# Kernel tuning notes

Measured on AMD Instinct MI355X. Metric: run time of the kernel, lower is better.

The kernel has to match this reference:

```python
import jax, jax.numpy as jnp
import numpy as np

PATCH = 3
PAD = PATCH // 2  # stride = 1


def _extract_patches(x):
    """torch F.unfold(k=3, s=1, p=1) reshaped to [b, n=h*w, c*3*3] (c slowest, then ki, kj)."""
    b, c, h, w = x.shape
    xp = jnp.pad(x, ((0, 0), (0, 0), (PAD, PAD), (PAD, PAD)))
    # stack the 9 shifted views -> [b, c, 9, h, w]
    pats = jnp.stack([xp[:, :, i:i + h, j:j + w]
                      for i in range(PATCH) for j in range(PATCH)], axis=2)
    pats = pats.reshape(b, c, PATCH, PATCH, h, w)
    # -> [b, h*w, c*PATCH*PATCH], matching torch unfold channel ordering
    return pats.transpose(0, 4, 5, 1, 2, 3).reshape(b, h * w, c * PATCH * PATCH)


def _l2_normalize(x):
    # F.normalize(dim=2): x / max(||x||_2, 1e-12)
    n = jnp.linalg.norm(x, axis=2, keepdims=True)
    return x / jnp.maximum(n, 1e-12)


def _fold(patches_flat, c, h, w):
    """torch F.fold(k=3, s=1, p=1): overlap-add patches back to [b, c, h, w]."""
    b = patches_flat.shape[0]
    p = patches_flat.reshape(b, h, w, c, PATCH, PATCH)
    out = jnp.zeros((b, c, h + 2 * PAD, w + 2 * PAD), patches_flat.dtype)
    for i in range(PATCH):
        for j in range(PATCH):
            out = out.at[:, :, i:i + h, j:j + w].add(
                p[:, :, :, :, i, j].transpose(0, 3, 1, 2))
    return out[:, :, PAD:PAD + h, PAD:PAD + w]


def setup_inputs() -> dict:
    key = jax.random.key(0)
    k1, k2 = jax.random.split(key)
    B, C, H, W = 1, 256, 96, 96
    return {
        "content_features": jax.random.normal(k1, (B, C, H, W), dtype=jnp.float32),
        "style_features": jax.random.normal(k2, (B, C, H, W), dtype=jnp.float32),
    }


def reference(content_features, style_features):
    b, c, h, w = content_features.shape
    cpat = _extract_patches(content_features)   # [b, n, d]
    spat = _extract_patches(style_features)     # [b, m, d]
    # all-pairs cosine similarity: [b, n, m]
    sim = jnp.einsum('bnd,bmd->bnm', _l2_normalize(cpat), _l2_normalize(spat))
    best = jnp.argmax(sim, axis=2)              # [b, n]
    matched = jnp.take_along_axis(spat, best[:, :, None], axis=1)  # [b, n, d]
    num = _fold(matched, c, h, w)
    den = _fold(jnp.ones_like(matched), c, h, w)
    return num / (den + 1e-8)
```

## Files before the change

kernel.cpp:

```cpp
#include <hip/hip_runtime.h>

#define HH 96
#define WW 96
#define CCH 256
#define NPIX (HH*WW)
#define HP 98
#define NROWS 9604
#define CORE_LO 99
#define CORE_HI 9505

typedef unsigned short u16;
typedef short bf16x8 __attribute__((ext_vector_type(8)));
typedef float f32x4 __attribute__((ext_vector_type(4)));
typedef int i32x4 __attribute__((ext_vector_type(4)));

__device__ __forceinline__ f32x4 ld4u(const float* p) {
    f32x4 r; __builtin_memcpy(&r, p, 16); return r;
}
__device__ __forceinline__ i32x4 ld4ui(const int* p) {
    i32x4 r; __builtin_memcpy(&r, p, 16); return r;
}

__device__ __forceinline__ u16 f2bf_rne(float x) {
    unsigned u = __float_as_uint(x);
    return (u16)((u + 0x7FFFu + ((u >> 16) & 1u)) >> 16);
}

__device__ __forceinline__ void stage8(const u16* const* srcs, u16* dst, int kb) {
#pragma unroll
    for (int t = 0; t < 8; ++t)
        __builtin_amdgcn_global_load_lds(
            (const __attribute__((address_space(1))) unsigned int*)(srcs[t] + kb),
            (__attribute__((address_space(3))) unsigned int*)(dst + t * 512),
            16, 0, 0);
}

__global__ __launch_bounds__(256) void tobf16_kernel(const float* __restrict__ X,
                                                     u16* __restrict__ HiT,
                                                     u16* __restrict__ LoT) {
    __shared__ u16 hi[64][65], lo[64][65];
    const int n0 = blockIdx.x * 64, k0 = blockIdx.y * 64;
    const int t = threadIdx.x;
    {
        const int kr = t >> 6, nl = t & 63;
#pragma unroll
        for (int r = 0; r < 16; ++r) {
            int kl = kr * 16 + r;
            float x = X[(k0 + kl) * NPIX + n0 + nl];
            u16 h = f2bf_rne(x);
            float hf = __uint_as_float((unsigned)h << 16);
            hi[kl][nl] = h;
            lo[kl][nl] = f2bf_rne(x - hf);
        }
    }
    __syncthreads();
    {
        const int nr = t >> 6, kl = t & 63;
#pragma unroll
        for (int r = 0; r < 16; ++r) {
            int nl = nr * 16 + r;
            HiT[(n0 + nl) * CCH + k0 + kl] = hi[kl][nl];
            LoT[(n0 + nl) * CCH + k0 + kl] = lo[kl][nl];
        }
    }
}

__global__ __launch_bounds__(256) void xst_kernel(const float* __restrict__ X,
                                                  float* __restrict__ XT) {
    __shared__ float tile[64][65];
    const int p0 = blockIdx.x * 64, c0 = blockIdx.y * 64;
    const int t = threadIdx.x;
    const int rr = t >> 6, cl = t & 63;
#pragma unroll
    for (int r = 0; r < 16; ++r)
        tile[rr * 16 + r][cl] = X[(c0 + rr * 16 + r) * NPIX + p0 + cl];
    __syncthreads();
#pragma unroll
    for (int r = 0; r < 16; ++r)
        XT[(p0 + rr * 16 + r) * CCH + c0 + cl] = tile[cl][rr * 16 + r];
}

__global__ __launch_bounds__(256) void prep_kernel(const float* __restrict__ Xs,
                                                   float* __restrict__ ssum,
                                                   unsigned long long* __restrict__ keys) {
    int p = blockIdx.x * 256 + threadIdx.x;
    if (p >= NPIX) return;
    float s = 0.f;
#pragma unroll 8
    for (int c = 0; c < CCH; ++c) {
        float v = Xs[c * NPIX + p];
        s = fmaf(v, v, s);
    }
    ssum[p] = s;
    keys[p] = 0ULL;
}

__global__ __launch_bounds__(256) void rnsbp_kernel(const float* __restrict__ ssum,
                                                    float* __restrict__ rnsp,
                                                    float* __restrict__ biasp,
                                                    int* __restrict__ midxp) {
    int mp = blockIdx.x * 256 + threadIdx.x;
    if (mp >= 9632) return;
    int yq = mp / HP, xq = mp - yq * HP;
    bool real = (yq >= 1 && yq <= 96 && xq >= 1 && xq <= 96);
    if (!real) { rnsp[mp] = 0.f; biasp[mp] = -3e38f; midxp[mp] = 0; return; }
    int y = yq - 1, x = xq - 1;
    float s = 0.f;
    for (int dy = -1; dy <= 1; ++dy) {
        int yy = y + dy;
        if ((unsigned)yy >= HH) continue;
        for (int dx = -1; dx <= 1; ++dx) {
            int xx = x + dx;
            if ((unsigned)xx >= WW) continue;
            s += ssum[yy * WW + xx];
        }
    }
    rnsp[mp] = 1.f / fmaxf(sqrtf(s), 1e-12f);
    biasp[mp] = 0.f;
    midxp[mp] = y * WW + x;
}

__global__ __launch_bounds__(256) void padzero_kernel(float* __restrict__ cc, int wstride) {
    int p = blockIdx.x;
    int yq = p / HP, xq = p - yq * HP;
    if (yq >= 1 && yq <= 96 && xq >= 1 && xq <= 96) return;
    const f32x4 z = {0.f, 0.f, 0.f, 0.f};
    float* row = cc + (long long)p * wstride;
    for (int c = threadIdx.x * 4; c < wstride; c += 1024)
        *(f32x4*)&row[c] = z;
}

__global__ __launch_bounds__(256, 2) void cc_gemm_kernel(
        const u16* __restrict__ ChiT, const u16* __restrict__ CloT,
        const u16* __restrict__ ShiT, const u16* __restrict__ SloT,
        const u16* __restrict__ zbuf,
        float* __restrict__ cc, int csp, int wstride) {
    __shared__ u16 lds[2][4][8][64][8];

    const int tid = threadIdx.x;
    const int n0 = blockIdx.x * 128;
    const int m0 = blockIdx.y * 128;
    const int wave = tid >> 6, lane = tid & 63;
    const int wr = wave >> 1, wc = wave & 1;
    const int rlo = lane & 15, kseg = (lane >> 4) * 8;

    const u16* srcs[8];
    if (wave < 2) {
        const u16* base = (wave == 0) ? ChiT : CloT;
#pragma unroll
        for (int t = 0; t < 8; ++t)
            srcs[t] = base + (n0 + t * 16 + rlo) * CCH + kseg;
    } else {
        const u16* base = (wave == 2) ? ShiT : SloT;
#pragma unroll
        for (int t = 0; t < 8; ++t) {
            int qp = csp + m0 + t * 16 + rlo;
            int yq = qp / HP, xq = qp - yq * HP;
            bool ok = (qp < NROWS) && (yq >= 1 && yq <= 96 && xq >= 1 && xq <= 96);
            srcs[t] = ok ? (base + ((yq - 1) * WW + (xq - 1)) * CCH + kseg)
                         : (zbuf + kseg);
        }
    }
    u16* slab0 = &lds[0][wave][0][0][0];
    u16* slab1 = &lds[1][wave][0][0][0];

    f32x4 acc[4][4];
#pragma unroll
    for (int i = 0; i < 4; ++i)
#pragma unroll
        for (int j = 0; j < 4; ++j) acc[i][j] = (f32x4){0.f, 0.f, 0.f, 0.f};

    stage8(srcs, slab0, 0);
    __syncthreads();

    for (int kk = 0; kk < 8; ++kk) {
        const int cur = kk & 1;
        if (kk < 7) stage8(srcs, cur ? slab0 : slab1, (kk + 1) * 32);

        bf16x8 ah[4], al[4], bh[4], bl[4];
#pragma unroll
        for (int i = 0; i < 4; ++i) {
            ah[i] = *(const bf16x8*)&lds[cur][0][wr * 4 + i][lane][0];
            al[i] = *(const bf16x8*)&lds[cur][1][wr * 4 + i][lane][0];
            bh[i] = *(const bf16x8*)&lds[cur][2][wc * 4 + i][lane][0];
            bl[i] = *(const bf16x8*)&lds[cur][3][wc * 4 + i][lane][0];
        }
#pragma unroll
        for (int i = 0; i < 4; ++i)
#pragma unroll
            for (int j = 0; j < 4; ++j) {
                acc[i][j] = __builtin_amdgcn_mfma_f32_16x16x32_bf16(ah[i], bh[j], acc[i][j], 0, 0, 0);
                acc[i][j] = __builtin_amdgcn_mfma_f32_16x16x32_bf16(ah[i], bl[j], acc[i][j], 0, 0, 0);
                acc[i][j] = __builtin_amdgcn_mfma_f32_16x16x32_bf16(al[i], bh[j], acc[i][j], 0, 0, 0);
            }
        __syncthreads();
    }

    const int r0 = (lane >> 4) * 4;
    const int cl = lane & 15;
#pragma unroll
    for (int i = 0; i < 4; ++i) {
        const int prow = n0 + wr * 64 + i * 16 + r0;
#pragma unroll
        for (int r = 0; r < 4; ++r) {
            const int row = prow + r;
            const int pp = row + 2 * (row / WW) + CORE_LO;
            const long long base = (long long)pp * wstride + m0 + wc * 64 + cl;
#pragma unroll
            for (int j = 0; j < 4; ++j)
                cc[base + j * 16] = acc[i][j][r];
        }
    }
}

__global__ __launch_bounds__(256) void boxsum_kernel(
        const float* __restrict__ cc, const float* __restrict__ rnsp,
        const float* __restrict__ biasp, const int* __restrict__ midxp,
        unsigned long long* __restrict__ keys,
        int core0, int coreEnd, int csp, int wstride) {
    const int wave = threadIdx.x >> 6, lane = threadIdx.x & 63;
    const int n = blockIdx.x * 4 + wave;
    const int pp = n + 2 * (n / WW) + CORE_LO;
    const long long rowbase = (long long)pp * wstride - csp;
    const int W1 = wstride + 1;

    const int OFF[9] = {-99, -98, -97, -1, 0, 1, 97, 98, 99};
    const float* tp[9];
#pragma unroll
    for (int t = 0; t < 9; ++t)
        tp[t] = cc + rowbase + core0 + lane * 4 + (long long)OFF[t] * W1;

    float best = -1e30f;
    int bidx = 0;
    for (int mq = core0 + lane * 4; mq < coreEnd; mq += 256) {
        f32x4 s = {0.f, 0.f, 0.f, 0.f};
#pragma unroll
        for (int t = 0; t < 9; ++t) { s += ld4u(tp[t]); tp[t] += 256; }
        f32x4 rv = ld4u(rnsp + mq);
        f32x4 bv = ld4u(biasp + mq);
        i32x4 iv = ld4ui(midxp + mq);
#pragma unroll
        for (int sl = 0; sl < 4; ++sl) {
            float v = fmaf(s[sl], rv[sl], bv[sl]);
            if (mq + sl >= coreEnd) v = -3e38f;
            if (v > best) { best = v; bidx = iv[sl]; }
        }
    }
#pragma unroll
    for (int d = 32; d; d >>= 1) {
        float ov = __shfl_xor(best, d);
        int oi = __shfl_xor(bidx, d);
        if (ov > best || (ov == best && oi < bidx)) { best = ov; bidx = oi; }
    }
    if (lane == 0) {
        unsigned u = __float_as_uint(best);
        unsigned key = (u & 0x80000000u) ? ~u : (u | 0x80000000u);
        unsigned long long k64 = ((unsigned long long)key << 32)
                               | (unsigned long long)(0xFFFFFFFFu - (unsigned)bidx);
        atomicMax(&keys[n], k64);
    }
}

__global__ __launch_bounds__(256) void fold2_kernel(const float* __restrict__ XsT,
                                                    const unsigned long long* __restrict__ keys,
                                                    float* __restrict__ outT) {
    const int wave = threadIdx.x >> 6, lane = threadIdx.x & 63;
    const int p = blockIdx.x * 4 + wave;
    const int y = p / WW, x = p - y * WW;
    f32x4 num = {0.f, 0.f, 0.f, 0.f};
    int den = 0;
#pragma unroll
    for (int i = 0; i < 3; ++i) {
        int ny = y + 1 - i;
        if ((unsigned)ny >= HH) continue;
#pragma unroll
        for (int j = 0; j < 3; ++j) {
            int nx = x + 1 - j;
            if ((unsigned)nx >= WW) continue;
            den++;
            unsigned long long k64 = keys[ny * WW + nx];
            int mg = (int)(0xFFFFFFFFu - (unsigned)(k64 & 0xFFFFFFFFu));
            int my = mg / WW, mx = mg - my * WW;
            int sy = my + i - 1, sx = mx + j - 1;
            if ((unsigned)sy < HH && (unsigned)sx < WW)
                num += ld4u(XsT + (long long)(sy * WW + sx) * CCH + lane * 4);
        }
    }
    float inv = 1.f / ((float)den + 1e-8f);
    f32x4 o = {num[0] * inv, num[1] * inv, num[2] * inv, num[3] * inv};
    *(f32x4*)&outT[(long long)p * CCH + lane * 4] = o;
}

__global__ __launch_bounds__(256) void outtr_kernel(const float* __restrict__ outT,
                                                    float* __restrict__ out) {
    __shared__ float tile[64][65];
    const int p0 = blockIdx.x * 64, c0 = blockIdx.y * 64;
    const int t = threadIdx.x;
    const int rr = t >> 6, cl = t & 63;
#pragma unroll
    for (int r = 0; r < 16; ++r)
        tile[rr * 16 + r][cl] = outT[(long long)(p0 + rr * 16 + r) * CCH + c0 + cl];
    __syncthreads();
#pragma unroll
    for (int r = 0; r < 16; ++r)
        out[(long long)(c0 + rr * 16 + r) * NPIX + p0 + cl] = tile[cl][rr * 16 + r];
}

extern "C" void kernel_launch(void* const* d_in, const int* in_sizes, int n_in,
                              void* d_out, int out_size, void* d_ws, size_t ws_size,
                              hipStream_t stream) {
    (void)in_sizes; (void)n_in; (void)out_size;
    const float* Xc = (const float*)d_in[0];
    const float* Xs = (const float*)d_in[1];
    float* out = (float*)d_out;

    char* w = (char*)d_ws;
    unsigned long long* keys = (unsigned long long*)w;  w += (size_t)NPIX * 8;
    float* ssum  = (float*)w;                           w += (size_t)NPIX * 4;
    float* rnsp  = (float*)w;                           w += (size_t)9632 * 4;
    float* biasp = (float*)w;                           w += (size_t)9632 * 4;
    int*   midxp = (int*)w;                             w += (size_t)9632 * 4;
    u16*   zbuf  = (u16*)w;                             w += 1024;
    float* XsT   = (float*)w;                           w += (size_t)NPIX * CCH * 4;
    float* outT  = (float*)w;                           w += (size_t)NPIX * CCH * 4;
    u16* ChiT = (u16*)w;                                w += (size_t)NPIX * CCH * 2;
    u16* CloT = (u16*)w;                                w += (size_t)NPIX * CCH * 2;
    u16* ShiT = (u16*)w;                                w += (size_t)NPIX * CCH * 2;
    u16* SloT = (u16*)w;                                w += (size_t)NPIX * CCH * 2;
    float* ccbuf = (float*)w;
    const size_t fixed = (size_t)(w - (char*)d_ws);

    long long avail = (ws_size > fixed + 4096)
                        ? (long long)(ws_size - fixed - 4096) : 0;
    int wstride = (int)(((avail / ((long long)NROWS * 4)) / 128) * 128);
    if (wstride > 2560) wstride = 2560;
    if (wstride < 512) wstride = 512;
    const int McCore = wstride - 198;

    hipMemsetAsync(zbuf, 0, 1024, stream);
    dim3 gt(NPIX / 64, CCH / 64);
    tobf16_kernel<<<gt, 256, 0, stream>>>(Xc, ChiT, CloT);
    tobf16_kernel<<<gt, 256, 0, stream>>>(Xs, ShiT, SloT);
    xst_kernel<<<gt, 256, 0, stream>>>(Xs, XsT);
    prep_kernel<<<NPIX / 256, 256, 0, stream>>>(Xs, ssum, keys);
    rnsbp_kernel<<<38, 256, 0, stream>>>(ssum, rnsp, biasp, midxp);
    padzero_kernel<<<NROWS, 256, 0, stream>>>(ccbuf, wstride);

    for (int core0 = CORE_LO; core0 < CORE_HI; core0 += McCore) {
        int coreEnd = (core0 + McCore < CORE_HI) ? core0 + McCore : CORE_HI;
        int csp = core0 - 99;
        int ce = coreEnd + 99; if (ce > NROWS) ce = NROWS;
        int Wc = ce - csp;
        dim3 g(NPIX / 128, (Wc + 127) / 128);
        cc_gemm_kernel<<<g, 256, 0, stream>>>(ChiT, CloT, ShiT, SloT, zbuf,
                                              ccbuf, csp, wstride);
        boxsum_kernel<<<NPIX / 4, 256, 0, stream>>>(ccbuf, rnsp, biasp, midxp, keys,
                                                    core0, coreEnd, csp, wstride);
    }

    fold2_kernel<<<NPIX / 4, 256, 0, stream>>>(XsT, keys, outT);
    outtr_kernel<<<gt, 256, 0, stream>>>(outT, out);
}
```

Measured before the change: 452.5 us.

## Prefetch two K-steps ahead with explicit vmcnt waits and split barriers

Restructures the GEMM main loop so two stages are loaded before compute begins. Each step waits on vmcnt only for the older stage, reads LDS into registers, then barriers before issuing the next async stage8 into the freed slab. The goal is to overlap global-to-LDS loads with the MFMA work and to hide more latency. The cost is hand-placed waitcnt and sched barriers, which depend on stage8 issuing exactly 8 vm ops and could break if that count changes.

```diff
diff --git a/kernel.cpp b/kernel.cpp
--- a/kernel.cpp
+++ b/kernel.cpp
@@ -171,30 +171,49 @@
         for (int j = 0; j < 4; ++j) acc[i][j] = (f32x4){0.f, 0.f, 0.f, 0.f};
 
     stage8(srcs, slab0, 0);
-    __syncthreads();
-
-    for (int kk = 0; kk < 8; ++kk) {
-        const int cur = kk & 1;
-        if (kk < 7) stage8(srcs, cur ? slab0 : slab1, (kk + 1) * 32);
-
-        bf16x8 ah[4], al[4], bh[4], bl[4];
-#pragma unroll
-        for (int i = 0; i < 4; ++i) {
-            ah[i] = *(const bf16x8*)&lds[cur][0][wr * 4 + i][lane][0];
-            al[i] = *(const bf16x8*)&lds[cur][1][wr * 4 + i][lane][0];
-            bh[i] = *(const bf16x8*)&lds[cur][2][wc * 4 + i][lane][0];
-            bl[i] = *(const bf16x8*)&lds[cur][3][wc * 4 + i][lane][0];
-        }
-#pragma unroll
-        for (int i = 0; i < 4; ++i)
-#pragma unroll
-            for (int j = 0; j < 4; ++j) {
-                acc[i][j] = __builtin_amdgcn_mfma_f32_16x16x32_bf16(ah[i], bh[j], acc[i][j], 0, 0, 0);
-                acc[i][j] = __builtin_amdgcn_mfma_f32_16x16x32_bf16(ah[i], bl[j], acc[i][j], 0, 0, 0);
-                acc[i][j] = __builtin_amdgcn_mfma_f32_16x16x32_bf16(al[i], bh[j], acc[i][j], 0, 0, 0);
-            }
-        __syncthreads();
-    }
+    stage8(srcs, slab1, 32);
+
+#define READS(CUR)                                                          \
+    bf16x8 ah[4], al[4], bh[4], bl[4];                                      \
+    _Pragma("unroll")                                                       \
+    for (int i = 0; i < 4; ++i) {                                           \
+        ah[i] = *(const bf16x8*)&lds[CUR][0][wr * 4 + i][lane][0];          \
+        al[i] = *(const bf16x8*)&lds[CUR][1][wr * 4 + i][lane][0];          \
+        bh[i] = *(const bf16x8*)&lds[CUR][2][wc * 4 + i][lane][0];          \
+        bl[i] = *(const bf16x8*)&lds[CUR][3][wc * 4 + i][lane][0];          \
+    }
+
+#define MFMAS                                                               \
+    _Pragma("unroll")                                                       \
+    for (int i = 0; i < 4; ++i)                                             \
+        _Pragma("unroll")                                                   \
+        for (int j = 0; j < 4; ++j) {                                       \
+            acc[i][j] = __builtin_amdgcn_mfma_f32_16x16x32_bf16(ah[i], bh[j], acc[i][j], 0, 0, 0); \
+            acc[i][j] = __builtin_amdgcn_mfma_f32_16x16x32_bf16(ah[i], bl[j], acc[i][j], 0, 0, 0); \
+            acc[i][j] = __builtin_amdgcn_mfma_f32_16x16x32_bf16(al[i], bh[j], acc[i][j], 0, 0, 0); \
+        }
+
+#define KSTEP(KK, WN)                                                       \
+    {                                                                       \
+        asm volatile("s_waitcnt vmcnt(" #WN ")" ::: "memory");              \
+        __builtin_amdgcn_sched_barrier(0);                                  \
+        __builtin_amdgcn_s_barrier();                                       \
+        READS((KK) & 1)                                                     \
+        asm volatile("s_waitcnt lgkmcnt(0)" ::: "memory");                  \
+        __builtin_amdgcn_sched_barrier(0);                                  \
+        __builtin_amdgcn_s_barrier();                                       \
+        if ((KK) + 2 < 8)                                                   \
+            stage8(srcs, (((KK) & 1)) ? slab1 : slab0, ((KK) + 2) * 32);    \
+        __builtin_amdgcn_sched_barrier(0);                                  \
+        MFMAS                                                               \
+    }
+
+    KSTEP(0, 8) KSTEP(1, 8) KSTEP(2, 8) KSTEP(3, 8)
+    KSTEP(4, 8) KSTEP(5, 8) KSTEP(6, 8) KSTEP(7, 0)
+
+#undef KSTEP
+#undef MFMAS
+#undef READS
 
     const int r0 = (lane >> 4) * 4;
     const int cl = lane & 15;
```

Result: no change. 447.7 us (-1.0%).
